# Kernel tuning notes

Measured on AMD Instinct MI355X. Metric: run time of the kernel, lower is better.

The kernel has to match this reference:

```python
import jax, jax.numpy as jnp
import numpy as np

PERCENTAGE = 0.26
BN_EPS = 1e-5


def _conv1x1(x, w, b):
    # x: (B,C,H,W), w: (O,C), b: (O,)
    return jnp.einsum('bchw,oc->bohw', x, w) + b[None, :, None, None]


def _bn_train(x, gamma, beta):
    # BatchNorm2d in training mode: biased variance over (B,H,W) per channel
    mean = x.mean(axis=(0, 2, 3), keepdims=True)
    var = jnp.mean((x - mean) ** 2, axis=(0, 2, 3), keepdims=True)
    xhat = (x - mean) * jax.lax.rsqrt(var + BN_EPS)
    return xhat * gamma[None, :, None, None] + beta[None, :, None, None]


def _band_mask(w, max_w):
    # The two mask-construction loops in the torch code reduce to |i-j| < max_w
    idx = jnp.arange(w)
    return jnp.abs(idx[:, None] - idx[None, :]) < max_w  # (w, w) bool


def setup_inputs() -> dict:
    key = jax.random.key(0)
    ks = jax.random.split(key, 16)
    B, C, H, W = 2, 256, 64, 512
    s = 0.02  # weight scale to keep attention logits in a sane range
    return {
        'x1': jax.random.normal(ks[0], (B, C, H, W), jnp.float32),
        'x2': jax.random.normal(ks[1], (B, C, H, W), jnp.float32),
        'Qw': jax.random.normal(ks[2], (C, C), jnp.float32) * s,
        'Qb': jax.random.normal(ks[3], (C,), jnp.float32) * s,
        'Kw': jax.random.normal(ks[4], (C, C), jnp.float32) * s,
        'Kb': jax.random.normal(ks[5], (C,), jnp.float32) * s,
        'Vw': jax.random.normal(ks[6], (C, C), jnp.float32) * s,
        'Vb': jax.random.normal(ks[7], (C,), jnp.float32) * s,
        'Vg': jax.random.normal(ks[8], (C,), jnp.float32),
        'Vbeta': jax.random.normal(ks[9], (C,), jnp.float32),
        'Ww': jax.random.normal(ks[10], (C, C), jnp.float32) * s,
        'Wb': jax.random.normal(ks[11], (C,), jnp.float32) * s,
        'Wg': jax.random.normal(ks[12], (C,), jnp.float32),
        'Wbeta': jax.random.normal(ks[13], (C,), jnp.float32),
    }


def reference(x1, x2, Qw, Qb, Kw, Kb, Vw, Vb, Vg, Vbeta, Ww, Wb, Wg, Wbeta):
    b, c, h, w = x1.shape
    max_w = int(w * PERCENTAGE)
    mask = _band_mask(w, max_w)  # (w, w), broadcasts over (b*h) rows
    neg_inf = jnp.float32(-jnp.inf)

    def rows(x):  # (B,C,H,W) -> (B*H, W, C)
        return x.transpose(0, 2, 3, 1).reshape(b * h, w, c)

    q1 = rows(_conv1x1(x1, Qw, Qb))
    q2 = rows(_conv1x1(x2, Qw, Qb))
    k1 = rows(_conv1x1(x1, Kw, Kb))  # (B*H, W, C); contract over C below
    k2 = rows(_conv1x1(x2, Kw, Kb))
    v1 = rows(_bn_train(_conv1x1(x1, Vw, Vb), Vg, Vbeta))
    v2 = rows(_bn_train(_conv1x1(x2, Vw, Vb), Vg, Vbeta))

    def attend(q, k, v):
        scores = jnp.einsum('nqc,nkc->nqk', q, k)  # (B*H, W, W)
        scores = jnp.where(mask[None], scores, neg_inf)
        p = jax.nn.softmax(scores, axis=-1)
        return jnp.einsum('nqk,nkc->nqc', p, v)

    def cols(y):  # (B*H, W, C) -> (B,C,H,W)
        return y.reshape(b, h, w, c).transpose(0, 3, 1, 2)

    y1 = cols(attend(q1, k2, v2))
    y2 = cols(attend(q2, k1, v1))
    z1 = _bn_train(_conv1x1(y1, Ww, Wb), Wg, Wbeta) + x1
    z2 = _bn_train(_conv1x1(y2, Ww, Wb), Wg, Wbeta) + x2
    return (z1, z2)
```

## Files before the change

### kernel.cpp

```cpp
#include <hip/hip_runtime.h>

typedef unsigned short u16;
typedef short bfrag __attribute__((ext_vector_type(8)));
typedef float ffrag __attribute__((ext_vector_type(4)));
typedef u16 u16x4 __attribute__((ext_vector_type(4)));
typedef float f4 __attribute__((ext_vector_type(4)));

#define MFMA16(a,b,c) __builtin_amdgcn_mfma_f32_16x16x32_bf16((a),(b),(c),0,0,0)

#define WAITV(N) do { asm volatile("s_waitcnt vmcnt(" #N ")" ::: "memory"); \
                      __builtin_amdgcn_sched_barrier(0); } while(0)
#define RBAR()   do { __builtin_amdgcn_s_barrier(); \
                      __builtin_amdgcn_sched_barrier(0); } while(0)


__device__ __forceinline__ u16 f2bf(float f){
  union { float f; unsigned int i; } cv; cv.f = f;
  unsigned int x = cv.i;
  return (u16)((x + 0x7fffu + ((x >> 16) & 1u)) >> 16);
}
__device__ __forceinline__ float bf2f(u16 u){
  union { unsigned int i; float f; } cv;
  cv.i = ((unsigned int)u) << 16;
  return cv.f;
}
__device__ __forceinline__ unsigned cvtpk(float lo, float hi){
  unsigned r; asm("v_cvt_pk_bf16_f32 %0, %1, %2" : "=v"(r) : "v"(lo), "v"(hi)); return r;
}
__device__ __forceinline__ bfrag ldb(const u16* p){
  bfrag v; __builtin_memcpy(&v, p, 16); return v;
}
__device__ __forceinline__ void gload_lds16(const u16* g, u16* l){
  __builtin_amdgcn_global_load_lds(
      (const __attribute__((address_space(1))) unsigned int*)g,
      (__attribute__((address_space(3))) unsigned int*)l, 16, 0, 0);
}

__global__ __launch_bounds__(256) void k_wcvt(const float* __restrict__ qw, const float* __restrict__ kw,
                                              const float* __restrict__ vw, const float* __restrict__ ww,
                                              u16* __restrict__ out){
  int t = blockIdx.x*256 + threadIdx.x;
  out[t]        = f2bf(qw[t]);
  out[t+65536]  = f2bf(kw[t]);
  out[t+131072] = f2bf(vw[t]);
  out[t+196608] = f2bf(ww[t]);
}

__global__ __launch_bounds__(256) void k_g(const float* __restrict__ Qb, const u16* __restrict__ wb,
                                           float* __restrict__ g){
  int t = threadIdx.x;
  float sm = 0.f;
  #pragma unroll 8
  for (int o=0;o<256;++o) sm += Qb[o]*bf2f(wb[65536 + o*256 + t]);
  g[t] = sm;
}

__global__ __launch_bounds__(256) void k_mg(const u16* __restrict__ wb, u16* __restrict__ wm){
  int c = blockIdx.x, t = threadIdx.x;
  float sm = 0.f;
  #pragma unroll 8
  for (int o=0;o<256;++o) sm += bf2f(wb[o*256 + c]) * bf2f(wb[65536 + o*256 + t]);
  wm[t*256 + c] = f2bf(sm);
}

__global__ __launch_bounds__(256) void k_c2(const u16* __restrict__ xr1, const u16* __restrict__ xr2,
                                            const float* __restrict__ g, float* __restrict__ c2){
  __shared__ float gs[256];
  int t = threadIdx.x;
  gs[t] = g[t];
  __syncthreads();
  int s = blockIdx.y;
  const u16* xr = s ? xr2 : xr1;
  float* out = c2 + s*65536;
  int l = t & 63, w = t >> 6;
  int half = l >> 5, cl = l & 31;
  for (int it=0; it<16; ++it){
    int row = blockIdx.x*128 + w*32 + it*2 + half;
    bfrag v = ldb(xr + (size_t)row*256 + cl*8);
    float sm = 0.f;
    #pragma unroll
    for (int e=0;e<8;++e) sm += bf2f((u16)v[e]) * gs[cl*8 + e];
    sm += __shfl_xor(sm,1,64);  sm += __shfl_xor(sm,2,64);
    sm += __shfl_xor(sm,4,64);  sm += __shfl_xor(sm,8,64);
    sm += __shfl_xor(sm,16,64);
    if (cl==0) out[row] = sm;
  }
}

__global__ __launch_bounds__(256) void k_xpose(const float* __restrict__ x1, const float* __restrict__ x2,
                                               u16* __restrict__ xr1, u16* __restrict__ xr2){
  const float* x = blockIdx.z ? x2 : x1;
  u16* xr = blockIdx.z ? xr2 : xr1;
  __shared__ float T[64][65];
  int t = threadIdx.x;
  int p0 = blockIdx.x*64, c0 = blockIdx.y*64;
  int b = p0 >> 15, q0 = p0 & 32767;
  #pragma unroll
  for (int it=0; it<4; ++it){
    int cc = it*16 + (t>>4);
    int pi = (t&15)*4;
    ffrag v; __builtin_memcpy(&v, x + ((size_t)(b*256 + c0 + cc))*32768 + q0 + pi, 16);
    T[cc][pi+0]=v[0]; T[cc][pi+1]=v[1]; T[cc][pi+2]=v[2]; T[cc][pi+3]=v[3];
  }
  __syncthreads();
  int pi = t>>2, cj0 = (t&3)*16;
  u16 tmp[16];
  #pragma unroll
  for (int j=0;j<16;++j) tmp[j] = f2bf(T[cj0+j][pi]);
  __builtin_memcpy(xr + (size_t)(p0+pi)*256 + c0 + cj0, tmp, 32);
}

template<int NI>
__device__ __forceinline__ void stageT(const u16* __restrict__ src, int row0, int k0,
                                       u16* lds, int wid, int l){
  #pragma unroll
  for (int rr=0; rr<NI; ++rr){
    int off = rr*4096 + wid*1024 + l*16;
    int row = off>>7, inb = off&127;
    int srcb = inb ^ ((row&7)<<4);
    gload_lds16(src + (size_t)(row0+row)*256 + k0 + (srcb>>1),
                lds + ((rr*4096 + wid*1024)>>1));
  }
}

__global__ __launch_bounds__(256, 3) void k_qkv(const u16* __restrict__ xr1, const u16* __restrict__ xr2,
    const u16* __restrict__ wb, const u16* __restrict__ wm,
    const float* __restrict__ vb,
    u16* __restrict__ XM1, u16* __restrict__ V1,
    u16* __restrict__ XM2, u16* __restrict__ V2){
  __shared__ __align__(16) u16 As[2][8192];
  __shared__ __align__(16) u16 Bs[2][4096];
  int id = blockIdx.x;
  int xcd = id & 7, j = id >> 3;
  int pl = j >> 4, v = j & 15;
  int ptile = xcd*64 + pl;
  int ot = v & 3, r = v >> 2;
  int wgtV = r >> 1, s = r & 1;
  const u16* A = s ? xr2 : xr1;
  const u16* W = wgtV ? (wb + 131072) : wm;

  int t = threadIdx.x, wid = t>>6, l = t&63, lr = l&15, lg = l>>4;
  int p0 = ptile*128, o0 = ot*64;
  int wr = wid*32;
  int swz = (lr&7)<<4;

  stageT<4>(A, p0, 0,  As[0], wid, l);
  stageT<2>(W, o0, 0,  Bs[0], wid, l);
  stageT<4>(A, p0, 64, As[1], wid, l);
  stageT<2>(W, o0, 64, Bs[1], wid, l);

  const ffrag fz = {0.f,0.f,0.f,0.f};
  ffrag acc[2][4];
  #pragma unroll
  for (int i=0;i<2;++i){ acc[i][0]=fz; acc[i][1]=fz; acc[i][2]=fz; acc[i][3]=fz; }

  #pragma unroll
  for (int ks=0; ks<4; ++ks){
    if (ks < 3) { WAITV(6); } else { WAITV(0); }
    RBAR();
    const u16* as = As[ks&1];
    const u16* bs = Bs[ks&1];
    #pragma unroll
    for (int kc=0; kc<2; ++kc){
      int colb = (kc*64 + lg*16) ^ swz;
      bfrag af[2], bf[4];
      #pragma unroll
      for (int mt=0; mt<2; ++mt)
        af[mt] = ldb(as + (((wr + mt*16 + lr)*128 + colb)>>1));
      #pragma unroll
      for (int nt=0; nt<4; ++nt)
        bf[nt] = ldb(bs + (((nt*16 + lr)*128 + colb)>>1));
      if (!wgtV){
        #pragma unroll
        for (int mt=0; mt<2; ++mt)
          #pragma unroll
          for (int nt=0; nt<4; ++nt)
            acc[mt][nt] = MFMA16(bf[nt], af[mt], acc[mt][nt]);
      } else {
        #pragma unroll
        for (int mt=0; mt<2; ++mt)
          #pragma unroll
          for (int nt=0; nt<4; ++nt)
            acc[mt][nt] = MFMA16(af[mt], bf[nt], acc[mt][nt]);
      }
    }
    RBAR();
    if (ks < 2){
      stageT<4>(A, p0, (ks+2)*64, As[ks&1], wid, l);
      stageT<2>(W, o0, (ks+2)*64, Bs[ks&1], wid, l);
    }
  }

  if (!wgtV){
    u16* op = s ? XM2 : XM1;
    #pragma unroll
    for (int nt=0; nt<4; ++nt){
      int ob = o0 + nt*16 + lg*4;
      #pragma unroll
      for (int mt=0; mt<2; ++mt){
        int p = p0 + wr + mt*16 + lr;
        u16x4 vv;
        #pragma unroll
        for (int rr=0;rr<4;++rr) vv[rr] = f2bf(acc[mt][nt][rr]);
        *reinterpret_cast<u16x4*>(op + (size_t)p*256 + ob) = vv;
      }
    }
  } else {
    u16* Vt = s ? V2 : V1;
    #pragma unroll
    for (int nt=0; nt<4; ++nt){
      int oo = o0 + nt*16 + lr;
      float bsc = vb[oo];
      #pragma unroll
      for (int mt=0; mt<2; ++mt){
        int pr = p0 + wr + mt*16 + lg*4;
        int n = pr >> 9, w0 = pr & 511;
        u16x4 vv;
        #pragma unroll
        for (int rr=0;rr<4;++rr) vv[rr] = f2bf(acc[mt][nt][rr] + bsc);
        *reinterpret_cast<u16x4*>(Vt + ((size_t)(n*256 + oo))*512 + w0) = vv;
      }
    }
  }
}

__global__ __launch_bounds__(256, 2) void k_conv1(const u16* __restrict__ in1, const u16* __restrict__ in2,
    const u16* __restrict__ wp, const float* __restrict__ bias,
    u16* __restrict__ o1, u16* __restrict__ o2,
    float* __restrict__ psum, float* __restrict__ psq){
  __shared__ __align__(16) u16 As[2][8192];
  __shared__ __align__(16) u16 Bs[2][8192];
  int id = blockIdx.x;
  int xcd = id & 7, j = id >> 3;
  int pl = j>>2, v = j&3;
  int ptile = xcd*64 + pl;
  int ot = v & 1, s = v >> 1;
  const u16* A = s ? in2 : in1;
  u16* out = s ? o2 : o1;

  int t = threadIdx.x, wid = t>>6, l = t&63, lr = l&15, lg = l>>4;
  int p0 = ptile*128, o0 = ot*128;
  int wr = (wid>>1)*64, wc = (wid&1)*64;
  int swz = (lr&7)<<4;

  stageT<4>(A, p0, 0,  As[0], wid, l);
  stageT<4>(wp, o0, 0, Bs[0], wid, l);
  stageT<4>(A, p0, 64, As[1], wid, l);
  stageT<4>(wp, o0, 64,Bs[1], wid, l);

  const ffrag fz = {0.f,0.f,0.f,0.f};
  ffrag acc[4][4];
  #pragma unroll
  for (int i=0;i<4;++i){ acc[i][0]=fz; acc[i][1]=fz; acc[i][2]=fz; acc[i][3]=fz; }

  #pragma unroll
  for (int ks=0; ks<4; ++ks){
    if (ks < 3) { WAITV(8); } else { WAITV(0); }
    RBAR();
    const u16* as = As[ks&1];
    const u16* bs = Bs[ks&1];
    #pragma unroll
    for (int kc=0; kc<2; ++kc){
      int colb = (kc*64 + lg*16) ^ swz;
      bfrag af[4], bfm[4];
      #pragma unroll
      for (int mt=0; mt<4; ++mt)
        af[mt] = ldb(as + (((wr + mt*16 + lr)*128 + colb)>>1));
      #pragma unroll
      for (int nt=0; nt<4; ++nt)
        bfm[nt] = ldb(bs + (((wc + nt*16 + lr)*128 + colb)>>1));
      #pragma unroll
      for (int mt=0; mt<4; ++mt)
        #pragma unroll
        for (int nt=0; nt<4; ++nt)
          acc[mt][nt] = MFMA16(af[mt], bfm[nt], acc[mt][nt]);
    }
    RBAR();
    if (ks < 2){
      stageT<4>(A, p0, (ks+2)*64, As[ks&1], wid, l);
      stageT<4>(wp, o0, (ks+2)*64, Bs[ks&1], wid, l);
    }
  }

  float pv[4], qv[4];
  #pragma unroll
  for (int nt=0; nt<4; ++nt){ pv[nt]=0.f; qv[nt]=0.f; }
  #pragma unroll
  for (int nt=0; nt<4; ++nt){
    int oo = o0 + wc + nt*16 + lr;
    float bsc = bias[oo];
    #pragma unroll
    for (int mt=0; mt<4; ++mt){
      int pr = p0 + wr + mt*16 + lg*4;
      #pragma unroll
      for (int rr=0;rr<4;++rr){
        float val = acc[mt][nt][rr] + bsc;
        out[(size_t)(pr + rr)*256 + oo] = f2bf(val);
        pv[nt] += val; qv[nt] += val*val;
      }
    }
  }
  #pragma unroll
  for (int nt=0; nt<4; ++nt){
    float sv = pv[nt], sq = qv[nt];
    sv += __shfl_xor(sv,16,64); sv += __shfl_xor(sv,32,64);
    sq += __shfl_xor(sq,16,64); sq += __shfl_xor(sq,32,64);
    if (lg==0){
      int oo = o0 + wc + nt*16 + lr;
      int idx = ((s*256 + oo)<<10) + (ptile<<1) + (wr>>6);
      psum[idx] = sv; psq[idx] = sq;
    }
  }
}

__global__ __launch_bounds__(256) void k_vstat1(const u16* __restrict__ V1, const u16* __restrict__ V2,
                                                float* __restrict__ ps, float* __restrict__ pq){
  int s = blockIdx.z;
  const u16* Vt = s ? V2 : V1;
  int c = blockIdx.x, ch = blockIdx.y, t = threadIdx.x;
  const u16* base = Vt + ((size_t)((ch*16 + (t>>4))*256 + c))*512 + (t&15)*32;
  float sm=0.f, sq=0.f;
  #pragma unroll
  for (int j=0;j<4;++j){
    bfrag v = ldb(base + j*8);
    #pragma unroll
    for (int e=0;e<8;++e){ float f = bf2f((u16)v[e]); sm+=f; sq+=f*f; }
  }
  __shared__ float rs[256], rq[256];
  rs[t]=sm; rq[t]=sq; __syncthreads();
  for (int st=128; st>0; st>>=1){ if (t<st){ rs[t]+=rs[t+st]; rq[t]+=rq[t+st]; } __syncthreads(); }
  if (t==0){ ps[s*2048 + c*8+ch]=rs[0]; pq[s*2048 + c*8+ch]=rq[0]; }
}
__global__ __launch_bounds__(256) void k_vstat2(const float* __restrict__ ps, const float* __restrict__ pq,
                                                const float* __restrict__ g, const float* __restrict__ be,
                                                float* __restrict__ aVall, float* __restrict__ bVall){
  int s = blockIdx.x, c = threadIdx.x;
  float sm=0.f, sq=0.f;
  #pragma unroll
  for (int ch=0; ch<8; ++ch){ sm += ps[s*2048 + c*8+ch]; sq += pq[s*2048 + c*8+ch]; }
  float mean = sm*(1.f/65536.f);
  float var  = sq*(1.f/65536.f) - mean*mean;
  float aa = g[c]*rsqrtf(var + 1e-5f);
  aVall[s*256+c]=aa; bVall[s*256+c]=be[c]-aa*mean;
}

__device__ __forceinline__ void stageK(const u16* Kn, u16* kb, int kt, int wid, int l){
  #pragma unroll
  for (int c2=0; c2<2; ++c2){
    int off = wid*2048 + c2*1024 + l*16;
    int row = off>>9, inb = off&511;
    int src = inb ^ ((row&7)<<4);
    gload_lds16(Kn + (size_t)(kt*16+row)*256 + (src>>1), kb + wid*1024 + c2*512);
  }
}
__device__ __forceinline__ void stageV(const u16* Vn, u16* vb, int k0, int wid, int l){
  #pragma unroll
  for (int c4=0; c4<4; ++c4){
    int off = wid*4096 + c4*1024 + l*16;
    int crow = off>>6, slot = (off>>4)&3;
    int kk = slot ^ ((crow>>1)&3);
    gload_lds16(Vn + (size_t)crow*512 + k0 + (kk<<3), vb + ((wid*4096 + c4*1024)>>1));
  }
}

__global__ __launch_bounds__(256, 2) void k_attn(
    const u16* __restrict__ XM1, const u16* __restrict__ xr2, const u16* __restrict__ V2,
    const u16* __restrict__ XM2, const u16* __restrict__ xr1, const u16* __restrict__ V1,
    const float* __restrict__ aVall, const float* __restrict__ bVall,
    const float* __restrict__ c2all,
    u16* __restrict__ O1, u16* __restrict__ O2){
  __shared__ __align__(16) u16 KP[2][8192];
  __shared__ __align__(16) u16 VBs[2][8192];
  int t = threadIdx.x, wid = t>>6, l = t&63, lr = l&15, lg = l>>4;
  int id = blockIdx.x;
  int s = id >> 10;
  int r0 = id & 1023;
  int xcd = r0 & 7, s5 = r0 >> 3;
  int qb = s5 & 7, n = (xcd<<4) | (s5>>3);
  const u16* Q = s ? XM2 : XM1;
  const u16* K = s ? xr1 : xr2;
  const u16* V = s ? V1 : V2;
  const float* aV = aVall + (s ? 0 : 256);
  const float* bV = bVall + (s ? 0 : 256);
  const float* c2k = c2all + ((s^1)<<16) + n*512;
  u16* O = s ? O2 : O1;

  int q0 = qb*64, q0w = q0 + wid*16;
  int lo = q0 - 132; if (lo < 0) lo = 0;
  int hi = q0 + 195; if (hi > 511) hi = 511;
  int KTLO = (lo>>4) & ~1;
  int KTHI = (hi>>4) | 1;
  int nsteps = (KTHI - KTLO + 2) >> 1;

  const u16* Kn = K + (size_t)n*131072;
  const u16* Vn = V + (size_t)n*131072;

  bfrag qa[8];
  const u16* Qrow = Q + ((size_t)(n*512 + q0w + lr))*256 + lg*8;
  #pragma unroll
  for (int ks=0; ks<8; ++ks) qa[ks] = ldb(Qrow + ks*32);
  f4 c2A, c2B, c2An, c2Bn;
  {
    int colb0 = KTLO*16 + lg*4;
    c2A = *reinterpret_cast<const f4*>(c2k + colb0);
    c2B = *reinterpret_cast<const f4*>(c2k + colb0 + 16);
    c2An = c2A; c2Bn = c2B;
  }
  WAITV(0);

  stageK(Kn, KP[0],        KTLO+0, wid, l);
  stageK(Kn, KP[0]+4096,   KTLO+1, wid, l);
  stageV(Vn, VBs[0],       KTLO*16 + 0,  wid, l);
  stageK(Kn, KP[1],        KTLO+2, wid, l);
  stageK(Kn, KP[1]+4096,   KTLO+3, wid, l);
  stageV(Vn, VBs[1],       KTLO*16 + 32, wid, l);

  const ffrag fz = {0.f,0.f,0.f,0.f};
  ffrag o[16];
  #pragma unroll
  for (int i=0;i<16;++i) o[i] = fz;
  float lsum = 0.f;
  int q = q0w + lr;
  int s0l = lr + (lg&1)*32;
  bool hi2 = (lg & 2) != 0;
  int vswz = (lg ^ ((lr>>1)&3))<<3;

  #pragma unroll
  for (int sp=0; sp<12; ++sp){
    if (sp < nsteps){
      if (sp == 0) { WAITV(8); }
      else if (sp < nsteps-1) { WAITV(10); }
      else { WAITV(0); }
      RBAR();
      const u16* kp = KP[sp&1];
      const u16* vb = VBs[sp&1];

      ffrag sA = fz, sB = fz;
      #pragma unroll
      for (int ks=0; ks<8; ++ks){
        int boff = (ks*64 + lg*16) ^ ((lr&7)<<4);
        bfrag kfA = ldb(kp + ((lr*512 + boff)>>1));
        bfrag kfB = ldb(kp + 4096 + ((lr*512 + boff)>>1));
        sA = MFMA16(kfA, qa[ks], sA);
        sB = MFMA16(kfB, qa[ks], sB);
      }

      int baseA = q + 132 - ((KTLO + 2*sp)*16 + lg*4);
      #pragma unroll
      for (int r=0;r<4;++r){
        bool vA = (unsigned)(baseA - r)      < 265u;
        bool vB = (unsigned)(baseA - r - 16) < 265u;
        float eA = vA ? __expf(sA[r] + c2A[r]) : 0.f;
        float eB = vB ? __expf(sB[r] + c2B[r]) : 0.f;
        sA[r] = eA; sB[r] = eB; lsum += eA + eB;
      }

      unsigned pk0A = cvtpk(sA[0], sA[1]);
      unsigned pk1A = cvtpk(sA[2], sA[3]);
      unsigned pk0B = cvtpk(sB[0], sB[1]);
      unsigned pk1B = cvtpk(sB[2], sB[3]);
      unsigned a0 = (unsigned)__shfl((int)pk0A, s0l,    64);
      unsigned a1 = (unsigned)__shfl((int)pk1A, s0l,    64);
      unsigned a2 = (unsigned)__shfl((int)pk0A, s0l+16, 64);
      unsigned a3 = (unsigned)__shfl((int)pk1A, s0l+16, 64);
      unsigned b0 = (unsigned)__shfl((int)pk0B, s0l,    64);
      unsigned b1 = (unsigned)__shfl((int)pk1B, s0l,    64);
      unsigned b2 = (unsigned)__shfl((int)pk0B, s0l+16, 64);
      unsigned b3 = (unsigned)__shfl((int)pk1B, s0l+16, 64);
      unsigned pu[4];
      pu[0] = hi2 ? b0 : a0;  pu[1] = hi2 ? b1 : a1;
      pu[2] = hi2 ? b2 : a2;  pu[3] = hi2 ? b3 : a3;
      bfrag pa; __builtin_memcpy(&pa, pu, 16);

      #pragma unroll
      for (int ct=0; ct<16; ++ct){
        bfrag vf = ldb(vb + (ct*16 + lr)*32 + vswz);
        o[ct] = MFMA16(pa, vf, o[ct]);
      }

      if (sp+1 < nsteps){
        int colbN = (KTLO + 2*(sp+1))*16 + lg*4;
        c2An = *reinterpret_cast<const f4*>(c2k + colbN);
        c2Bn = *reinterpret_cast<const f4*>(c2k + colbN + 16);
      }
      RBAR();
      if (sp+2 < nsteps){
        stageK(Kn, KP[sp&1],      KTLO + 2*sp + 4, wid, l);
        stageK(Kn, KP[sp&1]+4096, KTLO + 2*sp + 5, wid, l);
        stageV(Vn, VBs[sp&1],     KTLO*16 + (sp+2)*32, wid, l);
      }
      c2A = c2An; c2B = c2Bn;
    }
  }

  lsum += __shfl_xor(lsum, 16, 64);
  lsum += __shfl_xor(lsum, 32, 64);
  float rinv = 1.f / lsum;
  float linv[4];
  #pragma unroll
  for (int r=0;r<4;++r) linv[r] = __shfl(rinv, (lg<<2)+r, 64);
  #pragma unroll
  for (int ct=0; ct<16; ++ct){
    int c = ct*16 + lr;
    float av = aV[c], bv = bV[c];
    #pragma unroll
    for (int r=0;r<4;++r)
      O[((size_t)(n*512 + q0w + lg*4 + r))*256 + c] = f2bf(av*(o[ct][r]*linv[r]) + bv);
  }
}

__global__ __launch_bounds__(256) void k_ustat2(const float* __restrict__ psum, const float* __restrict__ psq,
                                                const float* __restrict__ g, const float* __restrict__ be,
                                                float* __restrict__ aWall, float* __restrict__ bWall){
  int c = blockIdx.x, s = blockIdx.y, t = threadIdx.x;
  const float* ps = psum + (((size_t)s*256 + c)<<10);
  const float* pq = psq  + (((size_t)s*256 + c)<<10);
  float sm = ps[t] + ps[t+256] + ps[t+512] + ps[t+768];
  float sq = pq[t] + pq[t+256] + pq[t+512] + pq[t+768];
  __shared__ float rs[256], rq[256];
  rs[t]=sm; rq[t]=sq; __syncthreads();
  for (int st=128; st>0; st>>=1){ if (t<st){ rs[t]+=rs[t+st]; rq[t]+=rq[t+st]; } __syncthreads(); }
  if (t==0){
    float mean = rs[0]*(1.f/65536.f);
    float var  = rq[0]*(1.f/65536.f) - mean*mean;
    float aa = g[c]*rsqrtf(var + 1e-5f);
    aWall[s*256+c]=aa; bWall[s*256+c]=be[c]-aa*mean;
  }
}

__global__ __launch_bounds__(256) void k_final(const u16* __restrict__ u1, const u16* __restrict__ u2,
                                               const u16* __restrict__ xr1, const u16* __restrict__ xr2,
                                               const float* __restrict__ aWall, const float* __restrict__ bWall,
                                               float* __restrict__ z){
  int s = blockIdx.z;
  const u16* u  = s ? u2 : u1;
  const u16* xr = s ? xr2 : xr1;
  const float* aW = aWall + s*256;
  const float* bW = bWall + s*256;
  float* zb = z + (size_t)s*16777216;
  __shared__ u16 Tu[64][66], Tx[64][66];
  int t = threadIdx.x;
  int p0 = blockIdx.x*64, c0 = blockIdx.y*64;
  int b = p0>>15, q0 = p0&32767;
  #pragma unroll
  for (int it=0; it<4; ++it){
    int pi = it*16 + (t>>4);
    int cj = (t&15)*4;
    u16x4 vu; __builtin_memcpy(&vu, u  + (size_t)(p0+pi)*256 + c0 + cj, 8);
    u16x4 vx; __builtin_memcpy(&vx, xr + (size_t)(p0+pi)*256 + c0 + cj, 8);
    *reinterpret_cast<u16x4*>(&Tu[pi][cj]) = vu;
    *reinterpret_cast<u16x4*>(&Tx[pi][cj]) = vx;
  }
  __syncthreads();
  int qi4 = (t&15)*4;
  #pragma unroll
  for (int it=0; it<4; ++it){
    int cc = it*16 + (t>>4);
    float a = aW[c0+cc], bw = bW[c0+cc];
    f4 vz;
    #pragma unroll
    for (int j=0;j<4;++j)
      vz[j] = a*bf2f(Tu[qi4+j][cc]) + bw + bf2f(Tx[qi4+j][cc]);
    *reinterpret_cast<f4*>(zb + ((size_t)(b*256 + c0 + cc))*32768 + q0 + qi4) = vz;
  }
}

extern "C" void kernel_launch(void* const* d_in, const int* in_sizes, int n_in,
                              void* d_out, int out_size, void* d_ws, size_t ws_size,
                              hipStream_t stream) {
  const float* x1  = (const float*)d_in[0];
  const float* x2  = (const float*)d_in[1];
  const float* Qw  = (const float*)d_in[2];
  const float* Qb  = (const float*)d_in[3];
  const float* Kw  = (const float*)d_in[4];
  const float* Kb  = (const float*)d_in[5];
  const float* Vw  = (const float*)d_in[6];
  const float* Vb  = (const float*)d_in[7];
  const float* Vg  = (const float*)d_in[8];
  const float* Vbe = (const float*)d_in[9];
  const float* Ww  = (const float*)d_in[10];
  const float* Wb  = (const float*)d_in[11];
  const float* Wg  = (const float*)d_in[12];
  const float* Wbe = (const float*)d_in[13];
  (void)Kb;

  char* ws = (char*)d_ws;
  const size_t S = 33554432;
  u16* xr1 = (u16*)(ws + 0*S);
  u16* xr2 = (u16*)(ws + 1*S);
  u16* XM1 = (u16*)(ws + 2*S);
  u16* u1  = (u16*)(ws + 3*S);
  u16* XM2 = (u16*)(ws + 4*S);
  u16* u2  = (u16*)(ws + 5*S);
  u16* wb  = (u16*)(ws + 6*S);
  float* vec = (float*)(ws + 6*S + 524288);
  float* aVall = vec;
  float* bVall = vec + 512;
  float* aWall = vec + 1024;
  float* bWall = vec + 1536;
  float* vps   = vec + 2048;
  float* vpq   = vec + 6144;
  u16*   wm    = (u16*)(vec + 10240);
  float* g     = vec + 43008;
  float* c2all = vec + 43264;

  char* douts = (char*)d_out;
  u16* Vt1 = (u16*)douts;
  u16* Vt2 = (u16*)(douts + S);
  u16* O1  = (u16*)(douts + 2*S);
  u16* O2  = (u16*)(douts + 3*S);
  float* upsum = (float*)douts;
  float* upsq  = upsum + 524288;
  float* z = (float*)d_out;

  dim3 gt(1024, 4, 2);
  dim3 gc2(512, 2);
  dim3 gv(256, 8, 2);
  dim3 gu2(256, 2);

  k_wcvt<<<256, 256, 0, stream>>>(Qw, Kw, Vw, Ww, wb);
  k_g<<<1, 256, 0, stream>>>(Qb, wb, g);
  k_mg<<<256, 256, 0, stream>>>(wb, wm);
  k_xpose<<<gt, 256, 0, stream>>>(x1, x2, xr1, xr2);
  k_c2<<<gc2, 256, 0, stream>>>(xr1, xr2, g, c2all);
  k_qkv<<<8192, 256, 0, stream>>>(xr1, xr2, wb, wm, Vb, XM1, Vt1, XM2, Vt2);
  k_vstat1<<<gv, 256, 0, stream>>>(Vt1, Vt2, vps, vpq);
  k_vstat2<<<2, 256, 0, stream>>>(vps, vpq, Vg, Vbe, aVall, bVall);
  k_attn<<<2048, 256, 0, stream>>>(XM1, xr2, Vt2, XM2, xr1, Vt1, aVall, bVall, c2all, O1, O2);
  k_conv1<<<2048, 256, 0, stream>>>(O1, O2, wb + 196608, Wb, u1, u2, upsum, upsq);
  k_ustat2<<<gu2, 256, 0, stream>>>(upsum, upsq, Wg, Wbe, aWall, bWall);
  k_final<<<gt, 256, 0, stream>>>(u1, u2, xr1, xr2, aWall, bWall, z);
}
```

Before: 347.8 us.

## Use 16-key attention steps with 16x16x16 MFMA to drop P shuffles

The banded attention loop now processes one 16-key tile per step instead of two. The softmax probabilities feed directly into a 16x16x16 bf16 MFMA in their native accumulator layout, which removes the cross-lane shuffles and selects. LDS buffers shrink by half and launch bounds rise to 4 blocks per CU to raise occupancy. In exchange the loop runs twice as many steps, each with its own barriers, uses an older MFMA with half the K depth, and drops the full unroll, so overhead per step goes up.

Measured after the change: 427.3 us. +22.8%, slower.

```diff
diff --git a/kernel.cpp b/kernel.cpp
--- a/kernel.cpp
+++ b/kernel.cpp
@@ -2,11 +2,13 @@
 
 typedef unsigned short u16;
 typedef short bfrag __attribute__((ext_vector_type(8)));
+typedef short bfrag4 __attribute__((ext_vector_type(4)));
 typedef float ffrag __attribute__((ext_vector_type(4)));
 typedef u16 u16x4 __attribute__((ext_vector_type(4)));
 typedef float f4 __attribute__((ext_vector_type(4)));
 
-#define MFMA16(a,b,c) __builtin_amdgcn_mfma_f32_16x16x32_bf16((a),(b),(c),0,0,0)
+#define MFMA16(a,b,c)  __builtin_amdgcn_mfma_f32_16x16x32_bf16((a),(b),(c),0,0,0)
+#define MFMAK16(a,b,c) __builtin_amdgcn_mfma_f32_16x16x16bf16_1k((a),(b),(c),0,0,0)
 
 #define WAITV(N) do { asm volatile("s_waitcnt vmcnt(" #N ")" ::: "memory"); \
                       __builtin_amdgcn_sched_barrier(0); } while(0)
@@ -353,24 +355,24 @@
     gload_lds16(Kn + (size_t)(kt*16+row)*256 + (src>>1), kb + wid*1024 + c2*512);
   }
 }
-__device__ __forceinline__ void stageV(const u16* Vn, u16* vb, int k0, int wid, int l){
-  #pragma unroll
-  for (int c4=0; c4<4; ++c4){
-    int off = wid*4096 + c4*1024 + l*16;
-    int crow = off>>6, slot = (off>>4)&3;
-    int kk = slot ^ ((crow>>1)&3);
-    gload_lds16(Vn + (size_t)crow*512 + k0 + (kk<<3), vb + ((wid*4096 + c4*1024)>>1));
-  }
-}
-
-__global__ __launch_bounds__(256, 2) void k_attn(
+__device__ __forceinline__ void stageV16(const u16* Vn, u16* vb, int k0, int wid, int l){
+  #pragma unroll
+  for (int it=0; it<2; ++it){
+    int c = it*128 + wid*32 + (l>>1);
+    int quad = ((l & 1) ^ ((l>>3)&1)) << 1;
+    gload_lds16(Vn + (size_t)c*512 + k0 + (quad<<2),
+                vb + ((it*4096 + wid*1024)>>1));
+  }
+}
+
+__global__ __launch_bounds__(256, 4) void k_attn(
     const u16* __restrict__ XM1, const u16* __restrict__ xr2, const u16* __restrict__ V2,
     const u16* __restrict__ XM2, const u16* __restrict__ xr1, const u16* __restrict__ V1,
     const float* __restrict__ aVall, const float* __restrict__ bVall,
     const float* __restrict__ c2all,
     u16* __restrict__ O1, u16* __restrict__ O2){
-  __shared__ __align__(16) u16 KP[2][8192];
-  __shared__ __align__(16) u16 VBs[2][8192];
+  __shared__ __align__(16) u16 KP[2][4096];
+  __shared__ __align__(16) u16 VB[2][4096];
   int t = threadIdx.x, wid = t>>6, l = t&63, lr = l&15, lg = l>>4;
   int id = blockIdx.x;
   int s = id >> 10;
@@ -388,9 +390,8 @@
   int q0 = qb*64, q0w = q0 + wid*16;
   int lo = q0 - 132; if (lo < 0) lo = 0;
   int hi = q0 + 195; if (hi > 511) hi = 511;
-  int KTLO = (lo>>4) & ~1;
-  int KTHI = (hi>>4) | 1;
-  int nsteps = (KTHI - KTLO + 2) >> 1;
+  int KTLO = lo>>4, KTHI = hi>>4;
+  int nsteps = KTHI - KTLO + 1;
 
   const u16* Kn = K + (size_t)n*131072;
   const u16* Vn = V + (size_t)n*131072;
@@ -399,21 +400,12 @@
   const u16* Qrow = Q + ((size_t)(n*512 + q0w + lr))*256 + lg*8;
   #pragma unroll
   for (int ks=0; ks<8; ++ks) qa[ks] = ldb(Qrow + ks*32);
-  f4 c2A, c2B, c2An, c2Bn;
-  {
-    int colb0 = KTLO*16 + lg*4;
-    c2A = *reinterpret_cast<const f4*>(c2k + colb0);
-    c2B = *reinterpret_cast<const f4*>(c2k + colb0 + 16);
-    c2An = c2A; c2Bn = c2B;
-  }
-  WAITV(0);
-
-  stageK(Kn, KP[0],        KTLO+0, wid, l);
-  stageK(Kn, KP[0]+4096,   KTLO+1, wid, l);
-  stageV(Vn, VBs[0],       KTLO*16 + 0,  wid, l);
-  stageK(Kn, KP[1],        KTLO+2, wid, l);
-  stageK(Kn, KP[1]+4096,   KTLO+3, wid, l);
-  stageV(Vn, VBs[1],       KTLO*16 + 32, wid, l);
+  f4 c2A = *reinterpret_cast<const f4*>(c2k + KTLO*16 + lg*4);
+  f4 c2An = c2A;
+  stageK (Kn, KP[0], KTLO,        wid, l);
+  stageV16(Vn, VB[0], KTLO*16,     wid, l);
+  stageK (Kn, KP[1], KTLO+1,      wid, l);
+  stageV16(Vn, VB[1], KTLO*16+16,  wid, l);
 
   const ffrag fz = {0.f,0.f,0.f,0.f};
   ffrag o[16];
@@ -421,76 +413,50 @@
   for (int i=0;i<16;++i) o[i] = fz;
   float lsum = 0.f;
   int q = q0w + lr;
-  int s0l = lr + (lg&1)*32;
-  bool hi2 = (lg & 2) != 0;
-  int vswz = (lg ^ ((lr>>1)&3))<<3;
-
-  #pragma unroll
-  for (int sp=0; sp<12; ++sp){
-    if (sp < nsteps){
-      if (sp == 0) { WAITV(8); }
-      else if (sp < nsteps-1) { WAITV(10); }
-      else { WAITV(0); }
-      RBAR();
-      const u16* kp = KP[sp&1];
-      const u16* vb = VBs[sp&1];
-
-      ffrag sA = fz, sB = fz;
-      #pragma unroll
-      for (int ks=0; ks<8; ++ks){
-        int boff = (ks*64 + lg*16) ^ ((lr&7)<<4);
-        bfrag kfA = ldb(kp + ((lr*512 + boff)>>1));
-        bfrag kfB = ldb(kp + 4096 + ((lr*512 + boff)>>1));
-        sA = MFMA16(kfA, qa[ks], sA);
-        sB = MFMA16(kfB, qa[ks], sB);
-      }
-
-      int baseA = q + 132 - ((KTLO + 2*sp)*16 + lg*4);
-      #pragma unroll
-      for (int r=0;r<4;++r){
-        bool vA = (unsigned)(baseA - r)      < 265u;
-        bool vB = (unsigned)(baseA - r - 16) < 265u;
-        float eA = vA ? __expf(sA[r] + c2A[r]) : 0.f;
-        float eB = vB ? __expf(sB[r] + c2B[r]) : 0.f;
-        sA[r] = eA; sB[r] = eB; lsum += eA + eB;
-      }
-
-      unsigned pk0A = cvtpk(sA[0], sA[1]);
-      unsigned pk1A = cvtpk(sA[2], sA[3]);
-      unsigned pk0B = cvtpk(sB[0], sB[1]);
-      unsigned pk1B = cvtpk(sB[2], sB[3]);
-      unsigned a0 = (unsigned)__shfl((int)pk0A, s0l,    64);
-      unsigned a1 = (unsigned)__shfl((int)pk1A, s0l,    64);
-      unsigned a2 = (unsigned)__shfl((int)pk0A, s0l+16, 64);
-      unsigned a3 = (unsigned)__shfl((int)pk1A, s0l+16, 64);
-      unsigned b0 = (unsigned)__shfl((int)pk0B, s0l,    64);
-      unsigned b1 = (unsigned)__shfl((int)pk1B, s0l,    64);
-      unsigned b2 = (unsigned)__shfl((int)pk0B, s0l+16, 64);
-      unsigned b3 = (unsigned)__shfl((int)pk1B, s0l+16, 64);
-      unsigned pu[4];
-      pu[0] = hi2 ? b0 : a0;  pu[1] = hi2 ? b1 : a1;
-      pu[2] = hi2 ? b2 : a2;  pu[3] = hi2 ? b3 : a3;
-      bfrag pa; __builtin_memcpy(&pa, pu, 16);
-
-      #pragma unroll
-      for (int ct=0; ct<16; ++ct){
-        bfrag vf = ldb(vb + (ct*16 + lr)*32 + vswz);
-        o[ct] = MFMA16(pa, vf, o[ct]);
-      }
-
-      if (sp+1 < nsteps){
-        int colbN = (KTLO + 2*(sp+1))*16 + lg*4;
-        c2An = *reinterpret_cast<const f4*>(c2k + colbN);
-        c2Bn = *reinterpret_cast<const f4*>(c2k + colbN + 16);
-      }
-      RBAR();
-      if (sp+2 < nsteps){
-        stageK(Kn, KP[sp&1],      KTLO + 2*sp + 4, wid, l);
-        stageK(Kn, KP[sp&1]+4096, KTLO + 2*sp + 5, wid, l);
-        stageV(Vn, VBs[sp&1],     KTLO*16 + (sp+2)*32, wid, l);
-      }
-      c2A = c2An; c2B = c2Bn;
-    }
+  int vbase = lr*16 + ((lg ^ (((lr>>2)&1)<<1))<<2);
+
+  for (int sp=0; sp<nsteps; ++sp){
+    if (sp < nsteps-1) { WAITV(4); } else { WAITV(0); }
+    RBAR();
+    const u16* kp = KP[sp&1];
+    const u16* vb = VB[sp&1];
+    int kt = KTLO + sp;
+
+    ffrag sA = fz;
+    #pragma unroll
+    for (int ks=0; ks<8; ++ks){
+      int boff = (ks*64 + lg*16) ^ ((lr&7)<<4);
+      bfrag kf = ldb(kp + ((lr*512 + boff)>>1));
+      sA = MFMA16(kf, qa[ks], sA);
+    }
+
+    int baseA = q + 132 - (kt*16 + lg*4);
+    #pragma unroll
+    for (int r=0;r<4;++r){
+      bool vA = (unsigned)(baseA - r) < 265u;
+      float e = vA ? __expf(sA[r] + c2A[r]) : 0.f;
+      sA[r] = e; lsum += e;
+    }
+
+    unsigned pu[2];
+    pu[0] = cvtpk(sA[0], sA[1]);
+    pu[1] = cvtpk(sA[2], sA[3]);
+    bfrag4 pa; __builtin_memcpy(&pa, pu, 8);
+
+    #pragma unroll
+    for (int ct=0; ct<16; ++ct){
+      bfrag4 vf; __builtin_memcpy(&vf, vb + ct*256 + vbase, 8);
+      o[ct] = MFMAK16(pa, vf, o[ct]);
+    }
+
+    if (sp+1 < nsteps)
+      c2An = *reinterpret_cast<const f4*>(c2k + (kt+1)*16 + lg*4);
+    RBAR();
+    if (sp+2 < nsteps){
+      stageK (Kn, KP[sp&1], kt+2,        wid, l);
+      stageV16(Vn, VB[sp&1], (kt+2)*16,  wid, l);
+    }
+    c2A = c2An;
   }
 
   lsum += __shfl_xor(lsum, 16, 64);
```
